# Kernel optimization log

Hardware: AMD Instinct MI355X
Metric: run time of the kernel (lower is better)

Reference implementation:

```python
import jax, jax.numpy as jnp
import numpy as np

B = 32768
NUM_SPARSE = 26
VOCAB = 100000
EMB = 128
DENSE_IN = 13
N_FIELDS = NUM_SPARSE + 1  # 27
INTER_DIM = N_FIELDS * (N_FIELDS - 1) // 2  # 351
TOP_IN = EMB + INTER_DIM  # 479


def setup_inputs() -> dict:
    key = jax.random.key(0)
    ks = jax.random.split(key, 12)
    inp = {
        "dense_x": jax.random.normal(ks[0], (B, DENSE_IN), dtype=jnp.float32),
        "sparse_x": jax.random.randint(ks[1], (B, NUM_SPARSE), 0, VOCAB, dtype=jnp.int64),
        # embedding tables stacked: [F, V, D]
        "emb_tables": jax.random.normal(ks[2], (NUM_SPARSE, VOCAB, EMB), dtype=jnp.float32) * 0.02,
        # bottom MLP: dense_in -> 256 -> emb
        "bw1": jax.random.normal(ks[3], (DENSE_IN, 256), dtype=jnp.float32) * 0.1,
        "bb1": jnp.zeros((256,), dtype=jnp.float32),
        "bw2": jax.random.normal(ks[4], (256, EMB), dtype=jnp.float32) * 0.05,
        "bb2": jnp.zeros((EMB,), dtype=jnp.float32),
        # top MLP: top_in -> 128 -> 64 -> 1
        "tw1": jax.random.normal(ks[5], (TOP_IN, 128), dtype=jnp.float32) * 0.05,
        "tb1": jnp.zeros((128,), dtype=jnp.float32),
        "tw2": jax.random.normal(ks[6], (128, 64), dtype=jnp.float32) * 0.1,
        "tb2": jnp.zeros((64,), dtype=jnp.float32),
        "tw3": jax.random.normal(ks[7], (64, 1), dtype=jnp.float32) * 0.1,
        "tb3": jnp.zeros((1,), dtype=jnp.float32),
    }
    return inp


def reference(dense_x, sparse_x, emb_tables, bw1, bb1, bw2, bb2,
              tw1, tb1, tw2, tb2, tw3, tb3):
    # bottom MLP
    h = jax.nn.relu(dense_x @ bw1 + bb1)
    x_bottom = jax.nn.relu(h @ bw2 + bb2)  # [B, EMB]

    # multi-table embedding gather: [B, F_sparse, EMB]
    field_idx = jnp.arange(NUM_SPARSE)[None, :]  # [1, F]
    sparse_embs = emb_tables[field_idx, sparse_x]  # [B, F, EMB]

    combined = jnp.concatenate([x_bottom[:, None, :], sparse_embs], axis=1)  # [B, 27, EMB]

    # pairwise dot interactions, take strict upper triangle
    interactions = jnp.einsum("bfd,bgd->bfg", combined, combined)  # [B, 27, 27]
    rows, cols = np.triu_indices(N_FIELDS, k=1)
    x_int = interactions[:, rows, cols]  # [B, 351]

    x_final = jnp.concatenate([x_bottom, x_int], axis=-1)  # [B, 479]

    # top MLP
    t = jax.nn.relu(x_final @ tw1 + tb1)
    t = jax.nn.relu(t @ tw2 + tb2)
    logits = t @ tw3 + tb3  # [B, 1]
    return jax.nn.sigmoid(logits)
```

## Files before the change

kernel.cpp:

```cpp
#include <hip/hip_runtime.h>
#include <hip/hip_bf16.h>
#include <stdint.h>

#define NUM_SPARSE 26
#define VOCAB 100000
#define EMB 128
#define ROWS 32

typedef __attribute__((ext_vector_type(8))) short bf16x8;
typedef __attribute__((ext_vector_type(16))) float f32x16;

__device__ __forceinline__ unsigned short f2bf(float x) {
    union { float f; uint32_t u; } v; v.f = x;
    uint32_t u = v.u;
    return (unsigned short)((u + 0x7FFFu + ((u >> 16) & 1u)) >> 16);
}
__device__ __forceinline__ uint32_t pack2bf(float a, float b) {
    __hip_bfloat162 h2 = __float22bfloat162_rn(float2{a, b});
    union { __hip_bfloat162 h; uint32_t u; } v; v.h = h2;
    return v.u;
}

__device__ __forceinline__ int swz(int r, int c, int rowbytes) {
    int b = 2 * c;
    return r * rowbytes + (((b >> 4) ^ (r & 15)) << 4) + (b & 15);
}
__device__ __forceinline__ bf16x8 ldsA(const char* base, int m, int k0, int rowbytes) {
    int slot = (k0 >> 3) ^ (m & 15);
    return *(const bf16x8*)(base + m * rowbytes + slot * 16);
}

__global__ void prep_weights(const float* __restrict__ bw2, const float* __restrict__ tw1,
                             const float* __restrict__ tw2, unsigned short* __restrict__ ws) {
    int i = blockIdx.x * blockDim.x + threadIdx.x;
    if (i < 256 * 128) {
        int k = i >> 7, n = i & 127;
        ws[n * 256 + k] = f2bf(bw2[i]);
    } else if (i < 256 * 128 + 479 * 128) {
        int j = i - 256 * 128;
        int k = j >> 7, n = j & 127;
        ws[32768 + n * 480 + k] = f2bf(tw1[j]);
    } else if (i < 256 * 128 + 479 * 128 + 128) {
        int n = i - (256 * 128 + 479 * 128);
        ws[32768 + n * 480 + 479] = 0;
    } else if (i < 256 * 128 + 479 * 128 + 128 + 128 * 64) {
        int j = i - (256 * 128 + 479 * 128 + 128);
        int k = j >> 6, n = j & 63;
        ws[94208 + n * 128 + k] = f2bf(tw2[j]);
    }
}

#define GATHER(row, BUF)                                                               \
    {                                                                                  \
        _Pragma("unroll") for (int i = 0; i < 13; i++) {                               \
            int fld = 2 * i + hi;                                                      \
            int idx = __shfl(idxs[row], fld);                                          \
            BUF[i] = *(const float4*)(emb + ((size_t)fld * VOCAB + (size_t)idx) * EMB  \
                                      + 4 * lm);                                       \
        }                                                                              \
    }

#define CONSUME(ri, BUF)                                                               \
    {                                                                                  \
        int r = w * 8 + (ri);                                                          \
        {                                                                              \
            uint32_t v = *(const uint32_t*)(xf + swz(r, 2 * l, 1024));                 \
            *(uint32_t*)(Cb + 4 * l) = v;     \
        }                                                                              \
        _Pragma("unroll") for (int i = 0; i < 13; i++) {                               \
            int frow = 1 + 2 * i + hi;                                                 \
            uint32_t p0 = pack2bf(BUF[i].x, BUF[i].y);                                 \
            uint32_t p1 = pack2bf(BUF[i].z, BUF[i].w);                                 \
            char* dst = Cb + frow * 256 + ((((lm >> 1) ^ (frow & 15))) << 4)           \
                        + (lm & 1) * 8;                                                \
            *(uint32_t*)dst = p0;                                                      \
            *(uint32_t*)(dst + 4) = p1;                                                \
        }                                                                              \
        f32x16 acc = {0,0,0,0,0,0,0,0,0,0,0,0,0,0,0,0};                                \
        _Pragma("unroll") for (int kk = 0; kk < 8; kk++) {                             \
            int k0 = kk * 16 + hi * 8;                                                 \
            bf16x8 a = ldsA(Cb, lm, k0, 256);                                          \
            acc = __builtin_amdgcn_mfma_f32_32x32x16_bf16(a, a, acc, 0, 0, 0);         \
        }                                                                              \
        int n = lm;                                                                    \
        if (n >= 1 && n <= 26) {                                                       \
            _Pragma("unroll") for (int reg = 0; reg < 16; reg++) {                     \
                int m = (reg & 3) + 8 * (reg >> 2) + 4 * hi;                           \
                if (m < n) {                                                           \
                    int p = 26 * m - (m * (m - 1)) / 2 + (n - m - 1);                  \
                    *(unsigned short*)(xf + swz(r, 128 + p, 1024)) = f2bf(acc[reg]);   \
                }                                                                      \
            }                                                                          \
        }                                                                              \
    }

__global__ __launch_bounds__(256, 2) void dlrm_main(
    const float* __restrict__ dense, const int* __restrict__ sparse,
    const float* __restrict__ emb, const float* __restrict__ bw1,
    const float* __restrict__ bb1, const float* __restrict__ bb2,
    const float* __restrict__ tb1, const float* __restrict__ tb2,
    const float* __restrict__ tw3, const float* __restrict__ tb3,
    const unsigned short* __restrict__ wsw, float* __restrict__ out)
{
    __shared__ __align__(16) char smem[65536];
    const int t = threadIdx.x;
    const int w = t >> 6;
    const int l = t & 63;
    const int hi = l >> 5;
    const int lm = l & 31;
    const int r0 = blockIdx.x * ROWS;

    float* xd = (float*)smem;
    char* xf = smem + 32768;
    char* Cb = smem + w * 8192;

    int idxs[8];
#pragma unroll
    for (int ri = 0; ri < 8; ri++)
        idxs[ri] = (l < NUM_SPARSE)
            ? sparse[(size_t)(r0 + w * 8 + ri) * NUM_SPARSE + l] : 0;

    for (int i = t; i < ROWS * 13; i += 256) xd[i] = dense[r0 * 13 + i];
    for (int i = t; i < ROWS * 33; i += 256) {
        int r = i / 33, c = 479 + (i - r * 33);
        *(unsigned short*)(xf + swz(r, c, 1024)) = 0;
    }

    float4 bufA[13], bufB[13];
    GATHER(0, bufA);
    GATHER(1, bufB);
    __syncthreads();

    {
        char* hb = smem + 2048;
        int j = t;
        float w1r[13];
#pragma unroll
        for (int k = 0; k < 13; k++) w1r[k] = bw1[k * 256 + j];
        float b = bb1[j];
        for (int r = 0; r < ROWS; r++) {
            float acc = b;
#pragma unroll
            for (int k = 0; k < 13; k++) acc += xd[r * 13 + k] * w1r[k];
            *(unsigned short*)(hb + swz(r, j, 512)) = f2bf(fmaxf(acc, 0.f));
        }
    }
    __syncthreads();

    {
        const char* hb = smem + 2048;
        const unsigned short* bw2t = wsw;
        int n0 = w * 32;
        f32x16 acc = {0,0,0,0,0,0,0,0,0,0,0,0,0,0,0,0};
#pragma unroll
        for (int kk = 0; kk < 16; kk++) {
            int k0 = kk * 16 + hi * 8;
            bf16x8 a = ldsA(hb, lm, k0, 512);
            bf16x8 b = *(const bf16x8*)(bw2t + (n0 + lm) * 256 + k0);
            acc = __builtin_amdgcn_mfma_f32_32x32x16_bf16(a, b, acc, 0, 0, 0);
        }
        float bias = bb2[n0 + lm];
#pragma unroll
        for (int reg = 0; reg < 16; reg++) {
            int m = (reg & 3) + 8 * (reg >> 2) + 4 * hi;
            float v = fmaxf(acc[reg] + bias, 0.f);
            *(unsigned short*)(xf + swz(m, n0 + lm, 1024)) = f2bf(v);
        }
    }
    __syncthreads();

    CONSUME(0, bufA); GATHER(2, bufA);
    CONSUME(1, bufB); GATHER(3, bufB);
    CONSUME(2, bufA); GATHER(4, bufA);
    CONSUME(3, bufB); GATHER(5, bufB);
    CONSUME(4, bufA); GATHER(6, bufA);
    CONSUME(5, bufB); GATHER(7, bufB);
    CONSUME(6, bufA);
    CONSUME(7, bufB);
    __syncthreads();

    {
        const unsigned short* tw1t = wsw + 32768;
        int n0 = w * 32;
        f32x16 acc = {0,0,0,0,0,0,0,0,0,0,0,0,0,0,0,0};
#pragma unroll
        for (int kk = 0; kk < 30; kk++) {
            int k0 = kk * 16 + hi * 8;
            bf16x8 a = ldsA(xf, lm, k0, 1024);
            bf16x8 b = *(const bf16x8*)(tw1t + (n0 + lm) * 480 + k0);
            acc = __builtin_amdgcn_mfma_f32_32x32x16_bf16(a, b, acc, 0, 0, 0);
        }
        float bias = tb1[n0 + lm];
#pragma unroll
        for (int reg = 0; reg < 16; reg++) {
            int m = (reg & 3) + 8 * (reg >> 2) + 4 * hi;
            float v = fmaxf(acc[reg] + bias, 0.f);
            *(unsigned short*)(smem + swz(m, n0 + lm, 256)) = f2bf(v);
        }
    }
    __syncthreads();

    float* t2b = (float*)(smem + 8192);
    if (w < 2) {
        const unsigned short* tw2t = wsw + 32768 + 61440;
        int n0 = w * 32;
        f32x16 acc = {0,0,0,0,0,0,0,0,0,0,0,0,0,0,0,0};
#pragma unroll
        for (int kk = 0; kk < 8; kk++) {
            int k0 = kk * 16 + hi * 8;
            bf16x8 a = ldsA(smem, lm, k0, 256);
            bf16x8 b = *(const bf16x8*)(tw2t + (n0 + lm) * 128 + k0);
            acc = __builtin_amdgcn_mfma_f32_32x32x16_bf16(a, b, acc, 0, 0, 0);
        }
        float bias = tb2[n0 + lm];
#pragma unroll
        for (int reg = 0; reg < 16; reg++) {
            int m = (reg & 3) + 8 * (reg >> 2) + 4 * hi;
            t2b[m * 65 + n0 + lm] = fmaxf(acc[reg] + bias, 0.f);
        }
    }
    __syncthreads();

    if (t < ROWS) {
        float acc = tb3[0];
#pragma unroll
        for (int k = 0; k < 64; k++) acc += t2b[t * 65 + k] * tw3[k];
        out[r0 + t] = 1.f / (1.f + expf(-acc));
    }
}

extern "C" void kernel_launch(void* const* d_in, const int* in_sizes, int n_in,
                              void* d_out, int out_size, void* d_ws, size_t ws_size,
                              hipStream_t stream) {
    const float* dense = (const float*)d_in[0];
    const int*   sparse = (const int*)d_in[1];
    const float* emb   = (const float*)d_in[2];
    const float* bw1   = (const float*)d_in[3];
    const float* bb1   = (const float*)d_in[4];
    const float* bw2   = (const float*)d_in[5];
    const float* bb2   = (const float*)d_in[6];
    const float* tw1   = (const float*)d_in[7];
    const float* tb1   = (const float*)d_in[8];
    const float* tw2   = (const float*)d_in[9];
    const float* tb2   = (const float*)d_in[10];
    const float* tw3   = (const float*)d_in[11];
    const float* tb3   = (const float*)d_in[12];
    unsigned short* wsw = (unsigned short*)d_ws;
    float* out = (float*)d_out;

    hipLaunchKernelGGL(prep_weights, dim3(400), dim3(256), 0, stream, bw2, tw1, tw2, wsw);
    hipLaunchKernelGGL(dlrm_main, dim3(32768 / ROWS), dim3(256), 0, stream,
                       dense, sparse, emb, bw1, bb1, bb2, tb1, tb2, tw3, tb3, wsw, out);
}
```

Before: 101.9 us.

## Halve rows per block, switch MLPs to 16x16 MFMA, raise occupancy

Each block now handles 16 rows instead of 32, with shared memory cut to 44KB and launch bounds raised to 3 blocks per CU, aiming for more resident waves to hide embedding-gather latency. The bottom and top MLP GEMMs move from 32x32x16 to 16x16x32 MFMA tiles to fit the 16-row tile, and all four waves now take part in the second top layer. The gather/consume pipeline is reordered so each gather is issued just before the previous buffer is consumed. The bf16 pack helper is replaced with a manual rounding version. The trade-off is that weights are reloaded from global memory by twice as many blocks, and there are more per-block fixed costs.

```diff
diff --git a/kernel.cpp b/kernel.cpp
--- a/kernel.cpp
+++ b/kernel.cpp
@@ -5,9 +5,10 @@
 #define NUM_SPARSE 26
 #define VOCAB 100000
 #define EMB 128
-#define ROWS 32
+#define ROWS 16
 
 typedef __attribute__((ext_vector_type(8))) short bf16x8;
+typedef __attribute__((ext_vector_type(4))) float f32x4;
 typedef __attribute__((ext_vector_type(16))) float f32x16;
 
 __device__ __forceinline__ unsigned short f2bf(float x) {
@@ -16,9 +17,7 @@
     return (unsigned short)((u + 0x7FFFu + ((u >> 16) & 1u)) >> 16);
 }
 __device__ __forceinline__ uint32_t pack2bf(float a, float b) {
-    __hip_bfloat162 h2 = __float22bfloat162_rn(float2{a, b});
-    union { __hip_bfloat162 h; uint32_t u; } v; v.h = h2;
-    return v.u;
+    return (uint32_t)f2bf(a) | ((uint32_t)f2bf(b) << 16);
 }
 
 __device__ __forceinline__ int swz(int r, int c, int rowbytes) {
@@ -62,7 +61,7 @@
 
 #define CONSUME(ri, BUF)                                                               \
     {                                                                                  \
-        int r = w * 8 + (ri);                                                          \
+        int r = w * 4 + (ri);                                                          \
         {                                                                              \
             uint32_t v = *(const uint32_t*)(xf + swz(r, 2 * l, 1024));                 \
             *(uint32_t*)(Cb + 4 * l) = v;     \
@@ -94,7 +93,7 @@
         }                                                                              \
     }
 
-__global__ __launch_bounds__(256, 2) void dlrm_main(
+__global__ __launch_bounds__(256, 3) void dlrm_main(
     const float* __restrict__ dense, const int* __restrict__ sparse,
     const float* __restrict__ emb, const float* __restrict__ bw1,
     const float* __restrict__ bb1, const float* __restrict__ bb2,
@@ -102,23 +101,25 @@
     const float* __restrict__ tw3, const float* __restrict__ tb3,
     const unsigned short* __restrict__ wsw, float* __restrict__ out)
 {
-    __shared__ __align__(16) char smem[65536];
+    __shared__ __align__(16) char smem[45056];
     const int t = threadIdx.x;
     const int w = t >> 6;
     const int l = t & 63;
     const int hi = l >> 5;
     const int lm = l & 31;
+    const int l16 = l & 15;
+    const int q4 = l >> 4;
     const int r0 = blockIdx.x * ROWS;
 
     float* xd = (float*)smem;
-    char* xf = smem + 32768;
-    char* Cb = smem + w * 8192;
-
-    int idxs[8];
-#pragma unroll
-    for (int ri = 0; ri < 8; ri++)
+    char* xf = smem + 28672;
+    char* Cb = smem + w * 7168;
+
+    int idxs[4];
+#pragma unroll
+    for (int ri = 0; ri < 4; ri++)
         idxs[ri] = (l < NUM_SPARSE)
-            ? sparse[(size_t)(r0 + w * 8 + ri) * NUM_SPARSE + l] : 0;
+            ? sparse[(size_t)(r0 + w * 4 + ri) * NUM_SPARSE + l] : 0;
 
     for (int i = t; i < ROWS * 13; i += 256) xd[i] = dense[r0 * 13 + i];
     for (int i = t; i < ROWS * 33; i += 256) {
@@ -128,7 +129,6 @@
 
     float4 bufA[13], bufB[13];
     GATHER(0, bufA);
-    GATHER(1, bufB);
     __syncthreads();
 
     {
@@ -150,73 +150,75 @@
     {
         const char* hb = smem + 2048;
         const unsigned short* bw2t = wsw;
-        int n0 = w * 32;
-        f32x16 acc = {0,0,0,0,0,0,0,0,0,0,0,0,0,0,0,0};
-#pragma unroll
-        for (int kk = 0; kk < 16; kk++) {
-            int k0 = kk * 16 + hi * 8;
-            bf16x8 a = ldsA(hb, lm, k0, 512);
-            bf16x8 b = *(const bf16x8*)(bw2t + (n0 + lm) * 256 + k0);
-            acc = __builtin_amdgcn_mfma_f32_32x32x16_bf16(a, b, acc, 0, 0, 0);
-        }
-        float bias = bb2[n0 + lm];
-#pragma unroll
-        for (int reg = 0; reg < 16; reg++) {
-            int m = (reg & 3) + 8 * (reg >> 2) + 4 * hi;
-            float v = fmaxf(acc[reg] + bias, 0.f);
-            *(unsigned short*)(xf + swz(m, n0 + lm, 1024)) = f2bf(v);
-        }
-    }
-    __syncthreads();
-
-    CONSUME(0, bufA); GATHER(2, bufA);
-    CONSUME(1, bufB); GATHER(3, bufB);
-    CONSUME(2, bufA); GATHER(4, bufA);
-    CONSUME(3, bufB); GATHER(5, bufB);
-    CONSUME(4, bufA); GATHER(6, bufA);
-    CONSUME(5, bufB); GATHER(7, bufB);
-    CONSUME(6, bufA);
-    CONSUME(7, bufB);
+#pragma unroll
+        for (int it = 0; it < 2; it++) {
+            int n0 = w * 32 + it * 16;
+            f32x4 acc = {0, 0, 0, 0};
+#pragma unroll
+            for (int kk = 0; kk < 8; kk++) {
+                int k0 = kk * 32 + q4 * 8;
+                bf16x8 a = ldsA(hb, l16, k0, 512);
+                bf16x8 b = *(const bf16x8*)(bw2t + (n0 + l16) * 256 + k0);
+                acc = __builtin_amdgcn_mfma_f32_16x16x32_bf16(a, b, acc, 0, 0, 0);
+            }
+            float bias = bb2[n0 + l16];
+#pragma unroll
+            for (int reg = 0; reg < 4; reg++) {
+                int m = q4 * 4 + reg;
+                float v = fmaxf(acc[reg] + bias, 0.f);
+                *(unsigned short*)(xf + swz(m, n0 + l16, 1024)) = f2bf(v);
+            }
+        }
+    }
+    __syncthreads();
+
+    GATHER(1, bufB); CONSUME(0, bufA);
+    GATHER(2, bufA); CONSUME(1, bufB);
+    GATHER(3, bufB); CONSUME(2, bufA);
+    CONSUME(3, bufB);
     __syncthreads();
 
     {
         const unsigned short* tw1t = wsw + 32768;
-        int n0 = w * 32;
-        f32x16 acc = {0,0,0,0,0,0,0,0,0,0,0,0,0,0,0,0};
-#pragma unroll
-        for (int kk = 0; kk < 30; kk++) {
-            int k0 = kk * 16 + hi * 8;
-            bf16x8 a = ldsA(xf, lm, k0, 1024);
-            bf16x8 b = *(const bf16x8*)(tw1t + (n0 + lm) * 480 + k0);
-            acc = __builtin_amdgcn_mfma_f32_32x32x16_bf16(a, b, acc, 0, 0, 0);
-        }
-        float bias = tb1[n0 + lm];
-#pragma unroll
-        for (int reg = 0; reg < 16; reg++) {
-            int m = (reg & 3) + 8 * (reg >> 2) + 4 * hi;
-            float v = fmaxf(acc[reg] + bias, 0.f);
-            *(unsigned short*)(smem + swz(m, n0 + lm, 256)) = f2bf(v);
+#pragma unroll
+        for (int it = 0; it < 2; it++) {
+            int n0 = w * 32 + it * 16;
+            f32x4 acc = {0, 0, 0, 0};
+#pragma unroll
+            for (int kk = 0; kk < 15; kk++) {
+                int k0 = kk * 32 + q4 * 8;
+                bf16x8 a = ldsA(xf, l16, k0, 1024);
+                bf16x8 b = *(const bf16x8*)(tw1t + (n0 + l16) * 480 + k0);
+                acc = __builtin_amdgcn_mfma_f32_16x16x32_bf16(a, b, acc, 0, 0, 0);
+            }
+            float bias = tb1[n0 + l16];
+#pragma unroll
+            for (int reg = 0; reg < 4; reg++) {
+                int m = q4 * 4 + reg;
+                float v = fmaxf(acc[reg] + bias, 0.f);
+                *(unsigned short*)(smem + swz(m, n0 + l16, 256)) = f2bf(v);
+            }
         }
     }
     __syncthreads();
 
     float* t2b = (float*)(smem + 8192);
-    if (w < 2) {
-        const unsigned short* tw2t = wsw + 32768 + 61440;
-        int n0 = w * 32;
-        f32x16 acc = {0,0,0,0,0,0,0,0,0,0,0,0,0,0,0,0};
-#pragma unroll
-        for (int kk = 0; kk < 8; kk++) {
-            int k0 = kk * 16 + hi * 8;
-            bf16x8 a = ldsA(smem, lm, k0, 256);
-            bf16x8 b = *(const bf16x8*)(tw2t + (n0 + lm) * 128 + k0);
-            acc = __builtin_amdgcn_mfma_f32_32x32x16_bf16(a, b, acc, 0, 0, 0);
-        }
-        float bias = tb2[n0 + lm];
-#pragma unroll
-        for (int reg = 0; reg < 16; reg++) {
-            int m = (reg & 3) + 8 * (reg >> 2) + 4 * hi;
-            t2b[m * 65 + n0 + lm] = fmaxf(acc[reg] + bias, 0.f);
+    {
+        const unsigned short* tw2t = wsw + 94208;
+        int n0 = w * 16;
+        f32x4 acc = {0, 0, 0, 0};
+#pragma unroll
+        for (int kk = 0; kk < 4; kk++) {
+            int k0 = kk * 32 + q4 * 8;
+            bf16x8 a = ldsA(smem, l16, k0, 256);
+            bf16x8 b = *(const bf16x8*)(tw2t + (n0 + l16) * 128 + k0);
+            acc = __builtin_amdgcn_mfma_f32_16x16x32_bf16(a, b, acc, 0, 0, 0);
+        }
+        float bias = tb2[n0 + l16];
+#pragma unroll
+        for (int reg = 0; reg < 4; reg++) {
+            int m = q4 * 4 + reg;
+            t2b[m * 65 + n0 + l16] = fmaxf(acc[reg] + bias, 0.f);
         }
     }
     __syncthreads();
```

Result: slower. 128.1 us (+25.7%).
